# Optimization experiments

Hardware: AMD Instinct MI355X
Metric: run time of the kernel (lower is better)

Reference implementation:

```python
import jax, jax.numpy as jnp
import numpy as np

N_BLOCKS = 96
N = N_BLOCKS ** 2          # number of image blocks = n_blocks^2
D = 1024                   # feature dim (fixed by Linear(1024+1, 128))
EPS_COS = 1e-6             # eps of F.cosine_similarity
EPS_BN = 1e-5              # BatchNorm1d eps


def setup_inputs() -> dict:
    key = jax.random.key(0)
    ks = jax.random.split(key, 6)
    return {
        "features": jax.random.normal(ks[0], (N, D), dtype=jnp.float32),
        "scores": jax.random.uniform(ks[1], (N,), dtype=jnp.float32),
        "W1": jax.random.normal(ks[2], (D + 1, 128), dtype=jnp.float32) * 0.03,
        "b1": jnp.zeros((128,), jnp.float32),
        "g1": jnp.ones((128,), jnp.float32),
        "be1": jnp.zeros((128,), jnp.float32),
        "W2": jax.random.normal(ks[3], (128, 64), dtype=jnp.float32) * 0.08,
        "b2": jnp.zeros((64,), jnp.float32),
        "g2": jnp.ones((64,), jnp.float32),
        "be2": jnp.zeros((64,), jnp.float32),
        "W3": jax.random.normal(ks[4], (64, 1), dtype=jnp.float32) * 0.12,
        "b3": jnp.zeros((1,), jnp.float32),
    }


def _gaussian_similarity(features):
    # Vectorized form of the O(N^2) pairwise loop:
    #   cos_ij = <f_i, f_j> / max(|f_i||f_j|, eps)
    #   sigma^2 = D * (0.5 + 0.5 * cos)  ->  2*sigma^2 = D * (1 + cos)
    #   sim_ij = exp(-|f_i - f_j|^2 / (2*sigma^2)),  sim_ii = 1
    sq = jnp.sum(features * features, axis=-1)          # [N] squared norms
    gram = features @ features.T                          # [N, N] big GEMM
    norms = jnp.sqrt(sq)
    cos = gram / jnp.maximum(norms[:, None] * norms[None, :], EPS_COS)
    d2 = jnp.maximum(sq[:, None] + sq[None, :] - 2.0 * gram, 0.0)
    denom = jnp.maximum(jnp.float32(D) * (1.0 + cos), EPS_COS)
    sim = jnp.exp(-d2 / denom)
    eye = jnp.eye(sim.shape[0], dtype=bool)
    return jnp.where(eye, jnp.float32(1.0), sim)


def _bn_eval(h, gamma, beta):
    # BatchNorm1d in eval mode with init running stats (mean=0, var=1).
    return gamma * (h / jnp.sqrt(1.0 + EPS_BN)) + beta


def reference(features, scores, W1, b1, g1, be1, W2, b2, g2, be2, W3, b3):
    sim = _gaussian_similarity(features)                  # [N, N]
    x = jnp.concatenate([features, scores[:, None]], axis=1)  # [N, D+1]
    h = jax.nn.relu(_bn_eval(x @ W1 + b1, g1, be1))       # [N, 128]
    h = jax.nn.relu(_bn_eval(h @ W2 + b2, g2, be2))       # [N, 64]
    agg = jax.nn.sigmoid(h @ W3 + b3)[:, 0]               # [N]
    sim_mean = jnp.mean(sim, axis=1)                      # [N]
    # Torch broadcast [N,1] * [N] -> [N,N], then .mean() == mean(agg)*mean(sim_mean)
    return jnp.mean(agg) * jnp.mean(sim_mean)


if __name__ == "__main__":
    out = reference(**setup_inputs())
    print(out)
```

## Files before the change

kernel.cpp:

```cpp
#include <hip/hip_runtime.h>

#define N_IMG 9216
#define DFEAT 1024
#define NBP 36
#define NPAIR2 666

typedef __attribute__((ext_vector_type(8))) short short8;
typedef __attribute__((ext_vector_type(4))) float floatx4;
typedef __attribute__((ext_vector_type(16))) float floatx16;
typedef __attribute__((ext_vector_type(4))) int intx4;
typedef __attribute__((ext_vector_type(8))) int intx8;

#define C1F 0.0014088818759657845f
#define C2F 0.05308355472172724f

__device__ __forceinline__ void async_copy16(const void* g, void* l) {
  __builtin_amdgcn_global_load_lds((const __attribute__((address_space(1))) void*)g,
                                   (__attribute__((address_space(3))) void*)l,
                                   16, 0, 0);
}

__device__ __forceinline__ unsigned short f2bf(float x) {
  union { float f; unsigned u; } a; a.f = x;
  unsigned u = a.u;
  u += 0x7fffu + ((u >> 16) & 1u);
  return (unsigned short)(u >> 16);
}

__device__ __forceinline__ unsigned q4(float z) {
  unsigned sg = (__float_as_uint(z) >> 28) & 8u;
  float a = fabsf(z);
  unsigned c = (a < 0.25f) ? 0u : (a < 0.75f) ? 1u : (a < 1.25f) ? 2u :
               (a < 1.75f) ? 3u : (a < 2.5f)  ? 4u : (a < 3.5f)  ? 5u :
               (a < 5.0f)  ? 6u : 7u;
  return c | sg;
}
__device__ __forceinline__ unsigned short pk4(float4 v, float sc) {
  unsigned b0 = q4(v.x * sc) | (q4(v.y * sc) << 4);
  unsigned b1 = q4(v.z * sc) | (q4(v.w * sc) << 4);
  return (unsigned short)(b0 | (b1 << 8));
}

__global__ __launch_bounds__(256) void convert_prep(const float* __restrict__ f,
                                                    const float* __restrict__ W1,
                                                    unsigned char* __restrict__ fbT,
                                                    float* __restrict__ sL,
                                                    float* __restrict__ pL,
                                                    unsigned short* __restrict__ W1t,
                                                    double* __restrict__ sums,
                                                    unsigned* __restrict__ ctr) {
  int b = blockIdx.x, t = threadIdx.x;
  if (b < 2304) {
    int lane = t & 63, wave = t >> 6;
    int row = b * 4 + wave;
    const float4* src = (const float4*)f + (size_t)row * 256;
    float4 v0 = src[lane], v1 = src[64 + lane], v2 = src[128 + lane], v3 = src[192 + lane];
    float s = v0.x * v0.x + v0.y * v0.y + v0.z * v0.z + v0.w * v0.w
            + v1.x * v1.x + v1.y * v1.y + v1.z * v1.z + v1.w * v1.w
            + v2.x * v2.x + v2.y * v2.y + v2.z * v2.z + v2.w * v2.w
            + v3.x * v3.x + v3.y * v3.y + v3.z * v3.z + v3.w * v3.w;
#pragma unroll
    for (int off = 32; off > 0; off >>= 1) s += __shfl_xor(s, off, 64);
    float zsc = rsqrtf(s) * 32.f;
    unsigned short u0 = pk4(v0, zsc), u1 = pk4(v1, zsc),
                   u2 = pk4(v2, zsc), u3 = pk4(v3, zsc);
    unsigned char* tb = fbT + (size_t)(row >> 5) * 16384 + (row & 31) * 32 + (lane & 15) * 2;
    int ko = (lane >> 4) * 1024;
    *(unsigned short*)(tb + ko) = u0;
    *(unsigned short*)(tb + ko + 4096) = u1;
    *(unsigned short*)(tb + ko + 8192) = u2;
    *(unsigned short*)(tb + ko + 12288) = u3;
    if (lane == 0) {
      sL[row] = s * C1F;
      pL[row] = sqrtf(s) * C2F;
    }
  } else {
    int j = b - 2304;
    if (j == 0) {
      if (t < 2) sums[t] = 0.0;
      if (t == 2) *ctr = 0u;
    }
    for (int k = t; k < DFEAT; k += 256)
      W1t[(size_t)j * DFEAT + k] = f2bf(W1[(size_t)k * 128 + j]);
  }
}

__global__ __launch_bounds__(512, 2) void gram_sim(const unsigned char* __restrict__ fbT,
                                                   const float* __restrict__ sL,
                                                   const float* __restrict__ pL,
                                                   double* __restrict__ sums) {
  __shared__ __align__(16) unsigned char stg[2][65536];
  __shared__ float sA[256], pA[256], sB[256], pB[256];
  __shared__ float wpart[8];

  int bid = blockIdx.x, t = threadIdx.x, lane = t & 63, wave = t >> 6;
  int xcd = bid & 7, t8 = bid >> 3;
  int L = (xcd < 2 ? xcd * 84 : 168 + (xcd - 2) * 83) + t8;
  int rem = L, bcol = 0;
  while (rem > bcol) { rem -= (bcol + 1); bcol++; }
  int brow = rem;

  if (t < 256) { sA[t] = sL[brow * 256 + t]; pA[t] = pL[brow * 256 + t]; }
  else { int u = t & 255; sB[u] = sL[bcol * 256 + u]; pB[u] = pL[bcol * 256 + u]; }
  __syncthreads();

  const unsigned char* srcA = fbT + (size_t)(brow * 8 + wave) * 16384 + lane * 16;
  const unsigned char* srcB = fbT + (size_t)(bcol * 8 + wave) * 16384 + lane * 16;
  char* dstA = (char*)stg + wave * 4096 + lane * 16;
  char* dstB = (char*)stg + 32768 + wave * 4096 + lane * 16;

#define STAGE(buf, q)                                                     \
  {                                                                       \
    const int go = (q) * 4096, lo = (buf) * 65536;                        \
    async_copy16(srcA + go,        dstA + lo);                            \
    async_copy16(srcA + go + 1024, dstA + lo + 1024);                     \
    async_copy16(srcA + go + 2048, dstA + lo + 2048);                     \
    async_copy16(srcA + go + 3072, dstA + lo + 3072);                     \
    async_copy16(srcB + go,        dstB + lo);                            \
    async_copy16(srcB + go + 1024, dstB + lo + 1024);                     \
    async_copy16(srcB + go + 2048, dstB + lo + 2048);                     \
    async_copy16(srcB + go + 3072, dstB + lo + 3072);                     \
  }

  const int r32 = lane & 31, kh = lane >> 5;
  const int loff = r32 * 32 + kh * 16;
  const int wr = (wave & 1) * 128, wc = (wave >> 1) * 64;
  const char* aBase = (const char*)stg + ((wave & 1) * 4) * 4096 + loff;
  const char* bBase = (const char*)stg + 32768 + ((wave >> 1) * 2) * 4096 + loff;

  floatx16 acc[4][2];
#pragma unroll
  for (int mi = 0; mi < 4; mi++)
#pragma unroll
    for (int ni = 0; ni < 2; ni++)
#pragma unroll
      for (int e = 0; e < 16; e++) acc[mi][ni][e] = 0.f;

  union u8x { intx8 v8; intx4 q[2]; };
  u8x A8[4], B8[2];
#pragma unroll
  for (int mi = 0; mi < 4; mi++) A8[mi].q[1] = (intx4){0, 0, 0, 0};
#pragma unroll
  for (int ni = 0; ni < 2; ni++) B8[ni].q[1] = (intx4){0, 0, 0, 0};

  STAGE(0, 0)
  STAGE(1, 1)
#pragma unroll
  for (int q = 0; q < 4; q++) {
    if (q < 3) asm volatile("s_waitcnt vmcnt(8)" ::: "memory");
    else       asm volatile("s_waitcnt vmcnt(0)" ::: "memory");
    __builtin_amdgcn_s_barrier();
    __builtin_amdgcn_sched_barrier(0);
    const int cur = (q & 1) * 65536;
#pragma unroll
    for (int c = 0; c < 4; c++) {
      const int co = cur + c * 1024;
#pragma unroll
      for (int mi = 0; mi < 4; mi++)
        A8[mi].q[0] = *(const intx4*)(aBase + co + mi * 4096);
#pragma unroll
      for (int ni = 0; ni < 2; ni++)
        B8[ni].q[0] = *(const intx4*)(bBase + co + ni * 4096);
#pragma unroll
      for (int mi = 0; mi < 4; mi++)
#pragma unroll
        for (int ni = 0; ni < 2; ni++)
          acc[mi][ni] = __builtin_amdgcn_mfma_scale_f32_32x32x64_f8f6f4(
              A8[mi].v8, B8[ni].v8, acc[mi][ni], 4, 4,
              0, 0x7F7F7F7F, 0, 0x7F7F7F7F);
    }
    __builtin_amdgcn_sched_barrier(0);
    __builtin_amdgcn_s_barrier();
    __builtin_amdgcn_sched_barrier(0);
    if (q < 2) STAGE((q & 1), q + 2)
  }
#undef STAGE

  const bool diag = (brow == bcol);
  float lsum = 0.f;
#pragma unroll
  for (int ni = 0; ni < 2; ni++) {
    int j_loc = wc + ni * 32 + r32;
    float sj = sB[j_loc], pj = pB[j_loc];
#pragma unroll
    for (int mi = 0; mi < 4; mi++) {
      int rbase = wr + mi * 32 + 4 * kh;
#pragma unroll
      for (int reg = 0; reg < 16; reg++) {
        int i_loc = rbase + (reg & 3) + 8 * (reg >> 2);
        float g = acc[mi][ni][reg];
        float si = sA[i_loc], pi = pA[i_loc];
        float r = __builtin_amdgcn_rcpf(1024.f + g);
        float del = pi * pj;
        float gam = si + sj + del;
        float sim = __builtin_amdgcn_exp2f(fmaf(-1024.f, gam * r, del));
        if (!diag) {
          lsum += sim;
        } else {
          lsum += (i_loc < j_loc) ? 2.f * sim : (i_loc == j_loc ? 1.f : 0.f);
        }
      }
    }
  }
  if (!diag) lsum *= 2.f;
#pragma unroll
  for (int off = 32; off > 0; off >>= 1) lsum += __shfl_down(lsum, off, 64);
  if (lane == 0) wpart[wave] = lsum;
  __syncthreads();
  if (t == 0) {
    float bs = 0.f;
#pragma unroll
    for (int w = 0; w < 8; w++) bs += wpart[w];
    atomicAdd(&sums[0], (double)bs);
  }
}

__global__ __launch_bounds__(256) void mlp_full(const float* __restrict__ f,
                                                const unsigned short* __restrict__ W1t,
                                                const float* __restrict__ scores,
                                                const float* __restrict__ W1,
                                                const float* __restrict__ b1,
                                                const float* __restrict__ g1,
                                                const float* __restrict__ be1,
                                                const float* __restrict__ W2, const float* __restrict__ b2,
                                                const float* __restrict__ g2, const float* __restrict__ be2,
                                                const float* __restrict__ W3, const float* __restrict__ b3,
                                                double* __restrict__ sums,
                                                unsigned* __restrict__ ctr,
                                                float* __restrict__ out) {
  int r0 = blockIdx.x * 32;

  __shared__ __align__(16) float As32[32 * 64];
  __shared__ __align__(16) unsigned short Bs[128 * 64];
  __shared__ float h1s[32][128];
  __shared__ float h2s[32][65];
  __shared__ float sc[32], b1s[128], g1s[128], be1s[128], wls[128], ls[32];

  int t = threadIdx.x, lane = t & 63, wave = t >> 6;
  if (t < 32) sc[t] = scores[r0 + t];
  if (t < 128) {
    b1s[t] = b1[t]; g1s[t] = g1[t]; be1s[t] = be1[t];
    wls[t] = W1[(size_t)DFEAT * 128 + t];
  }

  floatx4 acc[4];
#pragma unroll
  for (int b = 0; b < 4; b++) acc[b] = (floatx4){0.f, 0.f, 0.f, 0.f};

  const int wr = (wave & 1) * 16, wc = (wave >> 1) * 64;

  for (int k0 = 0; k0 < DFEAT; k0 += 64) {
    __syncthreads();
    {
      int c = t, rA = c >> 4, p = c & 15, l = p ^ (rA & 15);
      async_copy16(f + (size_t)(r0 + rA) * DFEAT + k0 + l * 4, (char*)As32 + c * 16);
      c = t + 256; rA = c >> 4; p = c & 15; l = p ^ (rA & 15);
      async_copy16(f + (size_t)(r0 + rA) * DFEAT + k0 + l * 4, (char*)As32 + c * 16);
#pragma unroll
      for (int q = 0; q < 4; q++) {
        int cc = t + q * 256, rB = cc >> 3, pp = cc & 7, ll = pp ^ (rB & 7);
        async_copy16(W1t + (size_t)rB * DFEAT + k0 + ll * 8, (char*)Bs + cc * 16);
      }
    }
    __syncthreads();

    const int mrow = lane & 15;
#pragma unroll
    for (int ks = 0; ks < 2; ks++) {
      const int kq = ks * 32 + (lane >> 4) * 8;
      short8 a, b[4];
      {
        int row = wr + mrow;
        int l0 = kq >> 2;
        int p0 = l0 ^ (row & 15), p1 = (l0 + 1) ^ (row & 15);
        float4 f0 = *(const float4*)&As32[row * 64 + p0 * 4];
        float4 f1 = *(const float4*)&As32[row * 64 + p1 * 4];
        a[0] = (short)f2bf(f0.x); a[1] = (short)f2bf(f0.y);
        a[2] = (short)f2bf(f0.z); a[3] = (short)f2bf(f0.w);
        a[4] = (short)f2bf(f1.x); a[5] = (short)f2bf(f1.y);
        a[6] = (short)f2bf(f1.z); a[7] = (short)f2bf(f1.w);
      }
#pragma unroll
      for (int nt = 0; nt < 4; nt++) {
        int row = wc + nt * 16 + mrow;
        int p = (kq >> 3) ^ (row & 7);
        b[nt] = *(const short8*)&Bs[row * 64 + p * 8];
      }
#pragma unroll
      for (int nt = 0; nt < 4; nt++)
        acc[nt] = __builtin_amdgcn_mfma_f32_16x16x32_bf16(a, b[nt], acc[nt], 0, 0, 0);
    }
  }

  const float inv = 1.0f / sqrtf(1.0f + 1e-5f);
  const int rq = (lane >> 4) * 4, cn = lane & 15;
#pragma unroll
  for (int nt = 0; nt < 4; nt++) {
    int j = wc + nt * 16 + cn;
    float bj = b1s[j], gj = g1s[j] * inv, bej = be1s[j], wj = wls[j];
#pragma unroll
    for (int rr = 0; rr < 4; rr++) {
      int iL = wr + rq + rr;
      float pre = acc[nt][rr] + sc[iL] * wj + bj;
      h1s[iL][j] = fmaxf(gj * pre + bej, 0.f);
    }
  }
  __syncthreads();

  {
    int j = t & 63, rg = (t >> 6) * 8;
    float a2[8];
#pragma unroll
    for (int rr = 0; rr < 8; rr++) a2[rr] = 0.f;
    for (int k = 0; k < 128; k++) {
      float w = W2[k * 64 + j];
#pragma unroll
      for (int rr = 0; rr < 8; rr++) a2[rr] = fmaf(h1s[rg + rr][k], w, a2[rr]);
    }
    float scv = g2[j] * inv, bi = b2[j], be = be2[j];
#pragma unroll
    for (int rr = 0; rr < 8; rr++)
      h2s[rg + rr][j] = fmaxf(scv * (a2[rr] + bi) + be, 0.f);
  }
  __syncthreads();

  if (t < 32) {
    float z = b3[0];
#pragma unroll
    for (int k = 0; k < 64; k++) z = fmaf(h2s[t][k], W3[k], z);
    ls[t] = 1.f / (1.f + __expf(-z));
  }
  __syncthreads();
  if (t == 0) {
    float s = 0.f;
#pragma unroll
    for (int iL = 0; iL < 32; iL++) s += ls[iL];
    atomicAdd(&sums[1], (double)s);
    __threadfence();
    unsigned prev = atomicAdd(ctr, 1u);
    if (prev == 287u) {
      __threadfence();
      double s0 = ((volatile double*)sums)[0];
      double s1 = ((volatile double*)sums)[1];
      out[0] = (float)((s1 / (double)N_IMG) * (s0 / ((double)N_IMG * (double)N_IMG)));
    }
  }
}

extern "C" void kernel_launch(void* const* d_in, const int* in_sizes, int n_in,
                              void* d_out, int out_size, void* d_ws, size_t ws_size,
                              hipStream_t stream) {
  const float* f      = (const float*)d_in[0];
  const float* scores = (const float*)d_in[1];
  const float* W1 = (const float*)d_in[2];
  const float* b1 = (const float*)d_in[3];
  const float* g1 = (const float*)d_in[4];
  const float* be1 = (const float*)d_in[5];
  const float* W2 = (const float*)d_in[6];
  const float* b2 = (const float*)d_in[7];
  const float* g2 = (const float*)d_in[8];
  const float* be2 = (const float*)d_in[9];
  const float* W3 = (const float*)d_in[10];
  const float* b3 = (const float*)d_in[11];

  char* ws = (char*)d_ws;
  unsigned char* fbT  = (unsigned char*)ws;
  float* sL           = (float*)(ws + 4718592);
  float* pL           = (float*)(ws + 4755456);
  unsigned short* W1t = (unsigned short*)(ws + 4792320);
  double* sums        = (double*)(ws + 5054464);
  unsigned* ctr       = (unsigned*)(ws + 5054480);

  convert_prep<<<2432, 256, 0, stream>>>(f, W1, fbT, sL, pL, W1t, sums, ctr);
  gram_sim<<<NPAIR2, 512, 0, stream>>>(fbT, sL, pL, sums);
  mlp_full<<<288, 256, 0, stream>>>(f, W1t, scores, W1, b1, g1, be1,
                                    W2, b2, g2, be2, W3, b3, sums, ctr,
                                    (float*)d_out);
}
```

Before: 187.3 us.

## Shrink gram tiles to 128x128 with more blocks; double-buffer MLP loads

The gram/similarity kernel moves from 256x256 upper-triangular tiles (666 blocks, 512 threads, 128KB LDS) to 128x128 tiles (2628 blocks, 256 threads, 16KB LDS). The K loop now runs in 16 fine-grained steps with double buffering, and the XCD-aware block mapping is rebalanced. This targets better load balance and occupancy across CUs, at the cost of lower data reuse per tile and more global traffic. The MLP kernel also gains a two-stage async double-buffered pipeline so loads overlap with MFMA work.

After: 188.8 us. Within noise of the previous version (+0.8%).

```diff
diff --git a/kernel.cpp b/kernel.cpp
--- a/kernel.cpp
+++ b/kernel.cpp
@@ -2,8 +2,8 @@
 
 #define N_IMG 9216
 #define DFEAT 1024
-#define NBP 36
-#define NPAIR2 666
+#define NBR2 72
+#define NPAIR4 2628
 
 typedef __attribute__((ext_vector_type(8))) short short8;
 typedef __attribute__((ext_vector_type(4))) float floatx4;
@@ -85,94 +85,81 @@
   }
 }
 
-__global__ __launch_bounds__(512, 2) void gram_sim(const unsigned char* __restrict__ fbT,
+__global__ __launch_bounds__(256, 3) void gram_sim(const unsigned char* __restrict__ fbT,
                                                    const float* __restrict__ sL,
                                                    const float* __restrict__ pL,
                                                    double* __restrict__ sums) {
-  __shared__ __align__(16) unsigned char stg[2][65536];
-  __shared__ float sA[256], pA[256], sB[256], pB[256];
-  __shared__ float wpart[8];
+  __shared__ __align__(16) unsigned char stg[2][8192];
+  __shared__ float sA[128], pA[128], sB[128], pB[128];
+  __shared__ float wpart[4];
 
   int bid = blockIdx.x, t = threadIdx.x, lane = t & 63, wave = t >> 6;
-  int xcd = bid & 7, t8 = bid >> 3;
-  int L = (xcd < 2 ? xcd * 84 : 168 + (xcd - 2) * 83) + t8;
+  int xcd = bid & 7, ii = bid >> 3;
+  int L = (xcd < 4 ? xcd * 329 : 1316 + (xcd - 4) * 328) + ii;
   int rem = L, bcol = 0;
   while (rem > bcol) { rem -= (bcol + 1); bcol++; }
   int brow = rem;
 
-  if (t < 256) { sA[t] = sL[brow * 256 + t]; pA[t] = pL[brow * 256 + t]; }
-  else { int u = t & 255; sB[u] = sL[bcol * 256 + u]; pB[u] = pL[bcol * 256 + u]; }
-  __syncthreads();
-
-  const unsigned char* srcA = fbT + (size_t)(brow * 8 + wave) * 16384 + lane * 16;
-  const unsigned char* srcB = fbT + (size_t)(bcol * 8 + wave) * 16384 + lane * 16;
-  char* dstA = (char*)stg + wave * 4096 + lane * 16;
-  char* dstB = (char*)stg + 32768 + wave * 4096 + lane * 16;
-
-#define STAGE(buf, q)                                                     \
-  {                                                                       \
-    const int go = (q) * 4096, lo = (buf) * 65536;                        \
-    async_copy16(srcA + go,        dstA + lo);                            \
-    async_copy16(srcA + go + 1024, dstA + lo + 1024);                     \
-    async_copy16(srcA + go + 2048, dstA + lo + 2048);                     \
-    async_copy16(srcA + go + 3072, dstA + lo + 3072);                     \
-    async_copy16(srcB + go,        dstB + lo);                            \
-    async_copy16(srcB + go + 1024, dstB + lo + 1024);                     \
-    async_copy16(srcB + go + 2048, dstB + lo + 2048);                     \
-    async_copy16(srcB + go + 3072, dstB + lo + 3072);                     \
+  if (t < 128) { sA[t] = sL[brow * 128 + t]; pA[t] = pL[brow * 128 + t]; }
+  else { int u = t - 128; sB[u] = sL[bcol * 128 + u]; pB[u] = pL[bcol * 128 + u]; }
+  __syncthreads();
+
+  const unsigned char* srcA = fbT + (size_t)(brow * 4 + wave) * 16384 + lane * 16;
+  const unsigned char* srcB = fbT + (size_t)(bcol * 4 + wave) * 16384 + lane * 16;
+  char* dstA = (char*)stg + wave * 1024 + lane * 16;
+  char* dstB = (char*)stg + 4096 + wave * 1024 + lane * 16;
+
+#define STAGE(buf, kb)                                        \
+  {                                                           \
+    async_copy16(srcA + (kb) * 1024, dstA + (buf) * 8192);    \
+    async_copy16(srcB + (kb) * 1024, dstB + (buf) * 8192);    \
   }
 
   const int r32 = lane & 31, kh = lane >> 5;
   const int loff = r32 * 32 + kh * 16;
-  const int wr = (wave & 1) * 128, wc = (wave >> 1) * 64;
-  const char* aBase = (const char*)stg + ((wave & 1) * 4) * 4096 + loff;
-  const char* bBase = (const char*)stg + 32768 + ((wave >> 1) * 2) * 4096 + loff;
-
-  floatx16 acc[4][2];
-#pragma unroll
-  for (int mi = 0; mi < 4; mi++)
+  const int wr = (wave & 1) * 64, wc = (wave >> 1) * 64;
+  const char* aBase = (const char*)stg + (wr >> 5) * 1024 + loff;
+  const char* bBase = (const char*)stg + 4096 + (wc >> 5) * 1024 + loff;
+
+  floatx16 acc[2][2];
+#pragma unroll
+  for (int mi = 0; mi < 2; mi++)
 #pragma unroll
     for (int ni = 0; ni < 2; ni++)
 #pragma unroll
       for (int e = 0; e < 16; e++) acc[mi][ni][e] = 0.f;
 
   union u8x { intx8 v8; intx4 q[2]; };
-  u8x A8[4], B8[2];
-#pragma unroll
-  for (int mi = 0; mi < 4; mi++) A8[mi].q[1] = (intx4){0, 0, 0, 0};
+  u8x A8[2], B8[2];
+#pragma unroll
+  for (int mi = 0; mi < 2; mi++) A8[mi].q[1] = (intx4){0, 0, 0, 0};
 #pragma unroll
   for (int ni = 0; ni < 2; ni++) B8[ni].q[1] = (intx4){0, 0, 0, 0};
 
   STAGE(0, 0)
   STAGE(1, 1)
 #pragma unroll
-  for (int q = 0; q < 4; q++) {
-    if (q < 3) asm volatile("s_waitcnt vmcnt(8)" ::: "memory");
-    else       asm volatile("s_waitcnt vmcnt(0)" ::: "memory");
+  for (int kb = 0; kb < 16; kb++) {
+    if (kb < 15) asm volatile("s_waitcnt vmcnt(2)" ::: "memory");
+    else         asm volatile("s_waitcnt vmcnt(0)" ::: "memory");
     __builtin_amdgcn_s_barrier();
     __builtin_amdgcn_sched_barrier(0);
-    const int cur = (q & 1) * 65536;
-#pragma unroll
-    for (int c = 0; c < 4; c++) {
-      const int co = cur + c * 1024;
-#pragma unroll
-      for (int mi = 0; mi < 4; mi++)
-        A8[mi].q[0] = *(const intx4*)(aBase + co + mi * 4096);
+    const int cur = (kb & 1) * 8192;
+    A8[0].q[0] = *(const intx4*)(aBase + cur);
+    A8[1].q[0] = *(const intx4*)(aBase + cur + 1024);
+    B8[0].q[0] = *(const intx4*)(bBase + cur);
+    B8[1].q[0] = *(const intx4*)(bBase + cur + 1024);
+#pragma unroll
+    for (int mi = 0; mi < 2; mi++)
 #pragma unroll
       for (int ni = 0; ni < 2; ni++)
-        B8[ni].q[0] = *(const intx4*)(bBase + co + ni * 4096);
-#pragma unroll
-      for (int mi = 0; mi < 4; mi++)
-#pragma unroll
-        for (int ni = 0; ni < 2; ni++)
-          acc[mi][ni] = __builtin_amdgcn_mfma_scale_f32_32x32x64_f8f6f4(
-              A8[mi].v8, B8[ni].v8, acc[mi][ni], 4, 4,
-              0, 0x7F7F7F7F, 0, 0x7F7F7F7F);
-    }
+        acc[mi][ni] = __builtin_amdgcn_mfma_scale_f32_32x32x64_f8f6f4(
+            A8[mi].v8, B8[ni].v8, acc[mi][ni], 4, 4,
+            0, 0x7F7F7F7F, 0, 0x7F7F7F7F);
     __builtin_amdgcn_sched_barrier(0);
     __builtin_amdgcn_s_barrier();
     __builtin_amdgcn_sched_barrier(0);
-    if (q < 2) STAGE((q & 1), q + 2)
+    if (kb < 14) STAGE((kb & 1), kb + 2)
   }
 #undef STAGE
 
@@ -183,7 +170,7 @@
     int j_loc = wc + ni * 32 + r32;
     float sj = sB[j_loc], pj = pB[j_loc];
 #pragma unroll
-    for (int mi = 0; mi < 4; mi++) {
+    for (int mi = 0; mi < 2; mi++) {
       int rbase = wr + mi * 32 + 4 * kh;
 #pragma unroll
       for (int reg = 0; reg < 16; reg++) {
@@ -207,12 +194,8 @@
   for (int off = 32; off > 0; off >>= 1) lsum += __shfl_down(lsum, off, 64);
   if (lane == 0) wpart[wave] = lsum;
   __syncthreads();
-  if (t == 0) {
-    float bs = 0.f;
-#pragma unroll
-    for (int w = 0; w < 8; w++) bs += wpart[w];
-    atomicAdd(&sums[0], (double)bs);
-  }
+  if (t == 0)
+    atomicAdd(&sums[0], (double)(wpart[0] + wpart[1] + wpart[2] + wpart[3]));
 }
 
 __global__ __launch_bounds__(256) void mlp_full(const float* __restrict__ f,
@@ -230,8 +213,8 @@
                                                 float* __restrict__ out) {
   int r0 = blockIdx.x * 32;
 
-  __shared__ __align__(16) float As32[32 * 64];
-  __shared__ __align__(16) unsigned short Bs[128 * 64];
+  __shared__ __align__(16) float As32[2 * 32 * 64];
+  __shared__ __align__(16) unsigned short Bs[2 * 128 * 64];
   __shared__ float h1s[32][128];
   __shared__ float h2s[32][65];
   __shared__ float sc[32], b1s[128], g1s[128], be1s[128], wls[128], ls[32];
@@ -242,6 +225,7 @@
     b1s[t] = b1[t]; g1s[t] = g1[t]; be1s[t] = be1[t];
     wls[t] = W1[(size_t)DFEAT * 128 + t];
   }
+  __syncthreads();
 
   floatx4 acc[4];
 #pragma unroll
@@ -249,20 +233,32 @@
 
   const int wr = (wave & 1) * 16, wc = (wave >> 1) * 64;
 
-  for (int k0 = 0; k0 < DFEAT; k0 += 64) {
-    __syncthreads();
-    {
-      int c = t, rA = c >> 4, p = c & 15, l = p ^ (rA & 15);
-      async_copy16(f + (size_t)(r0 + rA) * DFEAT + k0 + l * 4, (char*)As32 + c * 16);
-      c = t + 256; rA = c >> 4; p = c & 15; l = p ^ (rA & 15);
-      async_copy16(f + (size_t)(r0 + rA) * DFEAT + k0 + l * 4, (char*)As32 + c * 16);
-#pragma unroll
-      for (int q = 0; q < 4; q++) {
-        int cc = t + q * 256, rB = cc >> 3, pp = cc & 7, ll = pp ^ (rB & 7);
-        async_copy16(W1t + (size_t)rB * DFEAT + k0 + ll * 8, (char*)Bs + cc * 16);
-      }
-    }
-    __syncthreads();
+#define MSTAGE(buf, kk)                                                     \
+  {                                                                         \
+    const int k0_ = (kk) * 64;                                              \
+    int c = t, rA = c >> 4, p = c & 15, l = p ^ (rA & 15);                  \
+    async_copy16(f + (size_t)(r0 + rA) * DFEAT + k0_ + l * 4,               \
+                 (char*)As32 + (buf) * 8192 + c * 16);                      \
+    c = t + 256; rA = c >> 4; p = c & 15; l = p ^ (rA & 15);                \
+    async_copy16(f + (size_t)(r0 + rA) * DFEAT + k0_ + l * 4,               \
+                 (char*)As32 + (buf) * 8192 + c * 16);                      \
+    _Pragma("unroll")                                                       \
+    for (int q2 = 0; q2 < 4; q2++) {                                        \
+      int cc = t + q2 * 256, rB = cc >> 3, pp = cc & 7, ll = pp ^ (rB & 7); \
+      async_copy16(W1t + (size_t)rB * DFEAT + k0_ + ll * 8,                 \
+                   (char*)Bs + (buf) * 16384 + cc * 16);                    \
+    }                                                                       \
+  }
+
+  MSTAGE(0, 0)
+  MSTAGE(1, 1)
+  for (int kk = 0; kk < 16; kk++) {
+    if (kk < 15) asm volatile("s_waitcnt vmcnt(6)" ::: "memory");
+    else         asm volatile("s_waitcnt vmcnt(0)" ::: "memory");
+    __builtin_amdgcn_s_barrier();
+    __builtin_amdgcn_sched_barrier(0);
+    const int bufF = (kk & 1) * 2048;
+    const int bufS = (kk & 1) * 8192;
 
     const int mrow = lane & 15;
 #pragma unroll
@@ -273,8 +269,8 @@
         int row = wr + mrow;
         int l0 = kq >> 2;
         int p0 = l0 ^ (row & 15), p1 = (l0 + 1) ^ (row & 15);
-        float4 f0 = *(const float4*)&As32[row * 64 + p0 * 4];
-        float4 f1 = *(const float4*)&As32[row * 64 + p1 * 4];
+        float4 f0 = *(const float4*)&As32[bufF + row * 64 + p0 * 4];
+        float4 f1 = *(const float4*)&As32[bufF + row * 64 + p1 * 4];
         a[0] = (short)f2bf(f0.x); a[1] = (short)f2bf(f0.y);
         a[2] = (short)f2bf(f0.z); a[3] = (short)f2bf(f0.w);
         a[4] = (short)f2bf(f1.x); a[5] = (short)f2bf(f1.y);
@@ -284,13 +280,18 @@
       for (int nt = 0; nt < 4; nt++) {
         int row = wc + nt * 16 + mrow;
         int p = (kq >> 3) ^ (row & 7);
-        b[nt] = *(const short8*)&Bs[row * 64 + p * 8];
+        b[nt] = *(const short8*)&Bs[bufS + row * 64 + p * 8];
       }
 #pragma unroll
       for (int nt = 0; nt < 4; nt++)
         acc[nt] = __builtin_amdgcn_mfma_f32_16x16x32_bf16(a, b[nt], acc[nt], 0, 0, 0);
     }
-  }
+    __builtin_amdgcn_sched_barrier(0);
+    __builtin_amdgcn_s_barrier();
+    __builtin_amdgcn_sched_barrier(0);
+    if (kk < 14) MSTAGE((kk & 1), kk + 2)
+  }
+#undef MSTAGE
 
   const float inv = 1.0f / sqrtf(1.0f + 1e-5f);
   const int rq = (lane >> 4) * 4, cn = lane & 15;
@@ -372,7 +373,7 @@
   unsigned* ctr       = (unsigned*)(ws + 5054480);
 
   convert_prep<<<2432, 256, 0, stream>>>(f, W1, fbT, sL, pL, W1t, sums, ctr);
-  gram_sim<<<NPAIR2, 512, 0, stream>>>(fbT, sL, pL, sums);
+  gram_sim<<<NPAIR4, 256, 0, stream>>>(fbT, sL, pL, sums);
   mlp_full<<<288, 256, 0, stream>>>(f, W1t, scores, W1, b1, g1, be1,
                                     W2, b2, g2, be2, W3, b3, sums, ctr,
                                     (float*)d_out);
```
